# Kernel optimization log

Measured on AMD Instinct MI355X. Metric: run time of the kernel, lower is better.

## Reference

```python
import jax, jax.numpy as jnp
import numpy as np

N, K, C, OUT = 2048, 14, 512, 512
SCALE = 4.0
BN_EPS = 1e-5


def _edge_lists(k):
    # pairs i<j with i,j != k-1 and adj[i,j] > 0 (adj is fully connected ones)
    ei, ej = [], []
    for i in range(k - 1):
        for j in range(i + 1, k - 1):
            ei.append(i)
            ej.append(j)
    return np.asarray(ei, np.int32), np.asarray(ej, np.int32)


def setup_inputs() -> dict:
    key = jax.random.key(0)
    k0, k1, k2, k3 = jax.random.split(key, 4)
    ei, ej = _edge_lists(K)
    std = 0.02
    return {
        "inputs": jax.random.normal(k0, (N, K, C), dtype=jnp.float32),
        "adj": jnp.ones((K, K), dtype=jnp.float32),
        "edge_i": jnp.asarray(ei),
        "edge_j": jnp.asarray(ej),
        "gamma": jnp.ones((C,), dtype=jnp.float32),
        "beta": jnp.zeros((C,), dtype=jnp.float32),
        "w_direct": jax.random.normal(k1, (C,), dtype=jnp.float32) * std,
        "W_merged": jax.random.normal(k2, (OUT, C), dtype=jnp.float32) * std,
        "W_orig": jax.random.normal(k3, (OUT, C), dtype=jnp.float32) * std,
    }


def reference(inputs, adj, edge_i, edge_j, gamma, beta, w_direct, W_merged, W_orig):
    n, k, c = inputs.shape
    # --- learn_adj ---
    global_feat = inputs[:, k - 1 : k, :]                      # [N,1,c]
    distances = jnp.abs(inputs - global_feat)                  # [N,k,c]
    # pairwise gaps only on the static edge list (i<j, non-global, adj>0)
    gap = 15.0 * (distances[:, edge_i, :] - distances[:, edge_j, :])  # [N,E,c]
    # BatchNorm1d over channel c, batch stats over (N, E), biased variance
    mean = jnp.mean(gap, axis=(0, 1))
    var = jnp.mean(jnp.square(gap - mean), axis=(0, 1))
    bn = (gap - mean) * (gamma / jnp.sqrt(var + BN_EPS)) + beta        # [N,E,c]
    a = jax.nn.sigmoid(SCALE * jnp.einsum("nec,c->ne", bn, w_direct))  # [N,E]
    adj2 = jnp.ones((n, k, k), dtype=inputs.dtype)
    adj2 = adj2.at[:, edge_i, edge_j].set(2.0 * a)
    adj2 = adj2.at[:, edge_j, edge_i].set(2.0 * (1.0 - a))
    new_adj = adj2 * adj[None, :, :]
    norm = jnp.sum(jnp.abs(new_adj), axis=2, keepdims=True)    # L1 row norm
    new_adj = new_adj / jnp.maximum(norm, 1e-12)
    # --- graph conv ---
    agg = jnp.einsum("nij,njc->nic", new_adj, inputs)          # [N,k,c]
    merged = jax.nn.relu(jnp.einsum("nkc,oc->nko", agg, W_merged))
    original = jnp.einsum("nkc,oc->nko", inputs, W_orig)
    return merged + original
```

## Files before the change

kernel.cpp:

```cpp
#include <hip/hip_runtime.h>
#include <stdint.h>

#define K_NODES 14
#define C_DIM   512
#define OUT_DIM 512
#define N_EDGE  78

typedef float  f32x4  __attribute__((ext_vector_type(4)));
typedef __bf16 bf16x8 __attribute__((ext_vector_type(8)));

__device__ __forceinline__ unsigned short f2bf(float f) {
    unsigned int u = __builtin_bit_cast(unsigned int, f);
    unsigned int r = (u + 0x7fffu + ((u >> 16) & 1u)) >> 16;
    return (unsigned short)r;
}
__device__ __forceinline__ float bf2f(unsigned short s) {
    return __builtin_bit_cast(float, (unsigned int)s << 16);
}

__device__ __forceinline__ void async16(const void* g, void* l) {
    __builtin_amdgcn_global_load_lds(
        (const __attribute__((address_space(1))) unsigned int*)g,
        (__attribute__((address_space(3))) unsigned int*)l, 16, 0, 0);
}

__global__ __launch_bounds__(1024) void stats_partial(
    const float* __restrict__ x, float* __restrict__ part,
    unsigned short* __restrict__ xbf,
    const float* __restrict__ Wm, const float* __restrict__ Wo,
    unsigned short* __restrict__ wmbf, unsigned short* __restrict__ wobf)
{
    int t  = threadIdx.x;
    int q  = t & 127;
    int sn = t >> 7;
    int n  = blockIdx.x * 8 + sn;
    size_t base = (size_t)n * K_NODES * C_DIM + q * 4;

    f32x4 g = *(const f32x4*)(x + base + 13 * C_DIM);
    ushort4 gb; gb.x=f2bf(g.x); gb.y=f2bf(g.y); gb.z=f2bf(g.z); gb.w=f2bf(g.w);
    *(ushort4*)(xbf + base + 13 * C_DIM) = gb;

    float S10=0,S11=0,S12=0,S13=0, S20=0,S21=0,S22=0,S23=0, Sw0=0,Sw1=0,Sw2=0,Sw3=0;
    #pragma unroll
    for (int k = 0; k < 13; ++k) {
        f32x4 v = *(const f32x4*)(x + base + k * C_DIM);
        ushort4 vb; vb.x=f2bf(v.x); vb.y=f2bf(v.y); vb.z=f2bf(v.z); vb.w=f2bf(v.w);
        *(ushort4*)(xbf + base + k * C_DIM) = vb;
        float wk = (float)(12 - 2 * k);
        float d0=fabsf(v.x-g.x), d1=fabsf(v.y-g.y), d2=fabsf(v.z-g.z), d3=fabsf(v.w-g.w);
        S10+=d0; S11+=d1; S12+=d2; S13+=d3;
        S20+=d0*d0; S21+=d1*d1; S22+=d2*d2; S23+=d3*d3;
        Sw0+=wk*d0; Sw1+=wk*d1; Sw2+=wk*d2; Sw3+=wk*d3;
    }
    f32x4 as = (f32x4){15.f*Sw0, 15.f*Sw1, 15.f*Sw2, 15.f*Sw3};
    f32x4 aq = (f32x4){225.f*(13.f*S20 - S10*S10), 225.f*(13.f*S21 - S11*S11),
                       225.f*(13.f*S22 - S12*S12), 225.f*(13.f*S23 - S13*S13)};

    __shared__ f32x4 redS[8][128];
    __shared__ f32x4 redQ[8][128];
    redS[sn][q] = as;
    redQ[sn][q] = aq;
    __syncthreads();
    if (sn == 0) {
        f32x4 s = redS[0][q], z = redQ[0][q];
        #pragma unroll
        for (int r = 1; r < 8; ++r) { s += redS[r][q]; z += redQ[r][q]; }
        *(f32x4*)(part + (size_t)blockIdx.x * 1024 + q * 4)       = s;
        *(f32x4*)(part + (size_t)blockIdx.x * 1024 + 512 + q * 4) = z;
    }
    int i0 = blockIdx.x * 1024 + t;
    wmbf[i0] = f2bf(Wm[i0]);
    wobf[i0] = f2bf(Wo[i0]);
}

__global__ __launch_bounds__(256) void finalize_stats(
    const float* __restrict__ part, float inv_ne,
    const float* __restrict__ gamma, const float* __restrict__ beta,
    const float* __restrict__ wdir, float* __restrict__ u, float* __restrict__ bpart)
{
    int lane = threadIdx.x & 63;
    int wv   = threadIdx.x >> 6;
    int c    = blockIdx.x * 64 + lane;
    float s = 0.f, q = 0.f;
    #pragma unroll 8
    for (int r = wv; r < 256; r += 4) {
        s += part[(size_t)r * 1024 + c];
        q += part[(size_t)r * 1024 + 512 + c];
    }
    __shared__ float shs[4][64], shq[4][64];
    shs[wv][lane] = s; shq[wv][lane] = q;
    __syncthreads();
    if (wv == 0) {
        s = shs[0][lane] + shs[1][lane] + shs[2][lane] + shs[3][lane];
        q = shq[0][lane] + shq[1][lane] + shq[2][lane] + shq[3][lane];
        float mean = s * inv_ne;
        float var  = q * inv_ne - mean * mean;
        float sc   = gamma[c] / sqrtf(var + 1e-5f);
        u[c] = sc * wdir[c];
        float b = (beta[c] - mean * sc) * wdir[c];
        #pragma unroll
        for (int off = 1; off < 64; off <<= 1) b += __shfl_xor(b, off, 64);
        if (lane == 0) bpart[blockIdx.x] = b;
    }
}

__global__ __launch_bounds__(256) void fuse_graph(
    const unsigned short* __restrict__ xbf, const float* __restrict__ adj,
    const int* __restrict__ ei, const int* __restrict__ ej,
    const float* __restrict__ u, const float* __restrict__ bpart,
    unsigned short* __restrict__ aggbf)
{
    __shared__ float WL[2][196];
    __shared__ float Dp[2][2][13];
    __shared__ float invL[2][14];
    int wv = threadIdx.x >> 6, lane = threadIdx.x & 63;
    int sp = wv >> 1;
    int h  = wv & 1;
    int n  = blockIdx.x * 2 + sp;
    size_t base = (size_t)n * K_NODES * C_DIM + h * 256 + lane * 4;

    float xf[K_NODES][4];
    #pragma unroll
    for (int k = 0; k < K_NODES; ++k) {
        uint2 raw = *(const uint2*)(xbf + base + k * C_DIM);
        xf[k][0]=bf2f(raw.x&0xffff); xf[k][1]=bf2f(raw.x>>16);
        xf[k][2]=bf2f(raw.y&0xffff); xf[k][3]=bf2f(raw.y>>16);
    }
    f32x4 uv = *(const f32x4*)(u + h * 256 + lane * 4);

    #pragma unroll
    for (int k = 0; k < 13; ++k) {
        float p = fabsf(xf[k][0]-xf[13][0])*uv.x + fabsf(xf[k][1]-xf[13][1])*uv.y
                + fabsf(xf[k][2]-xf[13][2])*uv.z + fabsf(xf[k][3]-xf[13][3])*uv.w;
        #pragma unroll
        for (int off = 1; off < 64; off <<= 1) p += __shfl_xor(p, off, 64);
        if (lane == 0) Dp[sp][h][k] = p;
    }
    __syncthreads();

    if (h == 0) {
        float bc = 0.f;
        #pragma unroll
        for (int b8 = 0; b8 < 8; ++b8) bc += bpart[b8];
        for (int e = lane; e < N_EDGE; e += 64) {
            int ii = ei[e], jj = ej[e];
            float Di = Dp[sp][0][ii] + Dp[sp][1][ii];
            float Dj = Dp[sp][0][jj] + Dp[sp][1][jj];
            float z = 4.0f * (15.f * (Di - Dj) + bc);
            float a = 1.f / (1.f + expf(-z));
            WL[sp][ii * K_NODES + jj] = adj[ii * K_NODES + jj] * (2.f * a);
            WL[sp][jj * K_NODES + ii] = adj[jj * K_NODES + ii] * (2.f * (1.f - a));
        }
    } else {
        for (int idx = lane; idx < K_NODES * K_NODES; idx += 64) {
            int i = idx / K_NODES, j = idx - i * K_NODES;
            if (i == j || i == 13 || j == 13) WL[sp][idx] = adj[idx];
        }
    }
    __syncthreads();
    if (h == 0 && lane < K_NODES) {
        float s = 0.f;
        #pragma unroll
        for (int j = 0; j < K_NODES; ++j) s += fabsf(WL[sp][lane * K_NODES + j]);
        invL[sp][lane] = 1.f / fmaxf(s, 1e-12f);
    }
    __syncthreads();

    #pragma unroll
    for (int i = 0; i < K_NODES; ++i) {
        float s0=0.f,s1=0.f,s2=0.f,s3=0.f;
        #pragma unroll
        for (int j = 0; j < K_NODES; ++j) {
            float w = WL[sp][i * K_NODES + j];
            s0 += w*xf[j][0]; s1 += w*xf[j][1]; s2 += w*xf[j][2]; s3 += w*xf[j][3];
        }
        float wi = invL[sp][i];
        uint2 r;
        r.x = (unsigned int)f2bf(s0*wi) | ((unsigned int)f2bf(s1*wi) << 16);
        r.y = (unsigned int)f2bf(s2*wi) | ((unsigned int)f2bf(s3*wi) << 16);
        *(uint2*)(aggbf + base + i * C_DIM) = r;
    }
}

#define TM 128
#define TN 128
#define BK 64

__global__ __launch_bounds__(256) void gemm_fused(
    const unsigned short* __restrict__ Aagg, const unsigned short* __restrict__ Axin,
    const unsigned short* __restrict__ Bwm,  const unsigned short* __restrict__ Bwo,
    float* __restrict__ out)
{
    __shared__ unsigned short lA[2][TM * BK];
    __shared__ unsigned short lB[2][TN * BK];
    int tid  = threadIdx.x;
    int lane = tid & 63;
    int wave = tid >> 6;
    int wr = wave >> 1, wc = wave & 1;
    int bm = blockIdx.x * TM;
    int bn = blockIdx.y * TN;

    f32x4 acc[4][4];
    #pragma unroll
    for (int i = 0; i < 4; ++i)
        #pragma unroll
        for (int j = 0; j < 4; ++j) acc[i][j] = (f32x4){0.f, 0.f, 0.f, 0.f};

    int lrow = lane & 15;
    int xorv = lane & 7;
    int srow  = tid >> 3;
    int lcu   = ((tid & 7) ^ (srow & 7)) * 8;

#define STAGE(buf, Ap, Bp, kb)                                              \
    _Pragma("unroll")                                                        \
    for (int it = 0; it < 4; ++it) {                                         \
        int row = it * 32 + srow;                                            \
        async16((Ap) + (size_t)(bm + row) * C_DIM + (kb) + lcu,              \
                &lA[buf][(it * 256 + wave * 64) * 8]);                       \
        async16((Bp) + (size_t)(bn + row) * C_DIM + (kb) + lcu,              \
                &lB[buf][(it * 256 + wave * 64) * 8]);                       \
    }

    STAGE(0, Aagg, Bwm, 0);
    __syncthreads();

    #pragma unroll
    for (int ph = 0; ph < 16; ++ph) {
        const int cur = ph & 1;
        if (ph < 15) {
            const unsigned short* Ap = ((ph + 1) < 8) ? Aagg : Axin;
            const unsigned short* Bp = ((ph + 1) < 8) ? Bwm  : Bwo;
            STAGE(cur ^ 1, Ap, Bp, ((ph + 1) & 7) * BK);
        }
        #pragma unroll
        for (int ks = 0; ks < 2; ++ks) {
            int pchunk = ((ks * 4 + (lane >> 4)) ^ xorv) * 8;
            bf16x8 af[4], bfr[4];
            #pragma unroll
            for (int i = 0; i < 4; ++i)
                af[i] = *(const bf16x8*)&lA[cur][(wr * 64 + i * 16 + lrow) * BK + pchunk];
            #pragma unroll
            for (int j = 0; j < 4; ++j)
                bfr[j] = *(const bf16x8*)&lB[cur][(wc * 64 + j * 16 + lrow) * BK + pchunk];
            #pragma unroll
            for (int i = 0; i < 4; ++i)
                #pragma unroll
                for (int j = 0; j < 4; ++j)
                    acc[i][j] = __builtin_amdgcn_mfma_f32_16x16x32_bf16(
                        af[i], bfr[j], acc[i][j], 0, 0, 0);
        }
        if (ph == 7) {
            #pragma unroll
            for (int i = 0; i < 4; ++i)
                #pragma unroll
                for (int j = 0; j < 4; ++j)
                    #pragma unroll
                    for (int r = 0; r < 4; ++r)
                        acc[i][j][r] = fmaxf(acc[i][j][r], 0.f);
        }
        __syncthreads();
    }
#undef STAGE

    int orow0 = bm + wr * 64 + (lane >> 4) * 4;
    int ocol0 = bn + wc * 64 + (lane & 15);
    #pragma unroll
    for (int i = 0; i < 4; ++i)
        #pragma unroll
        for (int j = 0; j < 4; ++j)
            #pragma unroll
            for (int r = 0; r < 4; ++r)
                out[(size_t)(orow0 + i * 16 + r) * OUT_DIM + (ocol0 + j * 16)] = acc[i][j][r];
}

extern "C" void kernel_launch(void* const* d_in, const int* in_sizes, int n_in,
                              void* d_out, int out_size, void* d_ws, size_t ws_size,
                              hipStream_t stream)
{
    const float* x     = (const float*)d_in[0];
    const float* adj   = (const float*)d_in[1];
    const int*   ei    = (const int*)d_in[2];
    const int*   ej    = (const int*)d_in[3];
    const float* gamma = (const float*)d_in[4];
    const float* beta  = (const float*)d_in[5];
    const float* wdir  = (const float*)d_in[6];
    const float* Wm    = (const float*)d_in[7];
    const float* Wo    = (const float*)d_in[8];
    float* out = (float*)d_out;

    int N = in_sizes[0] / (K_NODES * C_DIM);
    int M = N * K_NODES;

    float* ws_f   = (float*)d_ws;
    float* u      = ws_f + 1024;
    float* bpart  = ws_f + 1536;
    float* part   = ws_f + 2048;
    char*  wsb    = (char*)d_ws;
    size_t off    = (size_t)(2048 + 256 * 1024) * sizeof(float);
    unsigned short* wmbf  = (unsigned short*)(wsb + off);  off += (size_t)OUT_DIM * C_DIM * 2;
    unsigned short* wobf  = (unsigned short*)(wsb + off);  off += (size_t)OUT_DIM * C_DIM * 2;
    unsigned short* xbf   = (unsigned short*)(wsb + off);  off += (size_t)M * C_DIM * 2;
    unsigned short* aggbf = (unsigned short*)(wsb + off);

    float inv_ne = 1.0f / ((float)N * (float)N_EDGE);

    hipLaunchKernelGGL(stats_partial, dim3(N / 8), dim3(1024), 0, stream,
                       x, part, xbf, Wm, Wo, wmbf, wobf);
    hipLaunchKernelGGL(finalize_stats, dim3(8), dim3(256), 0, stream,
                       part, inv_ne, gamma, beta, wdir, u, bpart);
    hipLaunchKernelGGL(fuse_graph, dim3(N / 2), dim3(256), 0, stream,
                       xbf, adj, ei, ej, u, bpart, aggbf);
    hipLaunchKernelGGL(gemm_fused, dim3(M / TM, OUT_DIM / TN), dim3(256), 0, stream,
                       aggbf, xbf, wmbf, wobf, out);
}
```

Baseline: 183.3 us.

## Rework stats/graph kernels' thread mapping and swizzle GEMM tile order

The stats kernel now uses 512 threads, each processing two samples, and converts twice as many weight elements. The graph kernel assigns one wave per sample with 8 channels per lane, which removes the block-level __syncthreads and the cross-wave partial sums. The GEMM launch becomes 1D with a remapped tile index that groups blocks by the 8 XCDs, for better L2 reuse of A rows. The main risks are lower occupancy from the larger register arrays and a hard-coded grid size (112) in the swizzle.

```diff
diff --git a/kernel.cpp b/kernel.cpp
--- a/kernel.cpp
+++ b/kernel.cpp
@@ -24,7 +24,7 @@
         (__attribute__((address_space(3))) unsigned int*)l, 16, 0, 0);
 }
 
-__global__ __launch_bounds__(1024) void stats_partial(
+__global__ __launch_bounds__(512) void stats_partial(
     const float* __restrict__ x, float* __restrict__ part,
     unsigned short* __restrict__ xbf,
     const float* __restrict__ Wm, const float* __restrict__ Wo,
@@ -33,44 +33,52 @@
     int t  = threadIdx.x;
     int q  = t & 127;
     int sn = t >> 7;
-    int n  = blockIdx.x * 8 + sn;
-    size_t base = (size_t)n * K_NODES * C_DIM + q * 4;
-
-    f32x4 g = *(const f32x4*)(x + base + 13 * C_DIM);
-    ushort4 gb; gb.x=f2bf(g.x); gb.y=f2bf(g.y); gb.z=f2bf(g.z); gb.w=f2bf(g.w);
-    *(ushort4*)(xbf + base + 13 * C_DIM) = gb;
-
-    float S10=0,S11=0,S12=0,S13=0, S20=0,S21=0,S22=0,S23=0, Sw0=0,Sw1=0,Sw2=0,Sw3=0;
-    #pragma unroll
-    for (int k = 0; k < 13; ++k) {
-        f32x4 v = *(const f32x4*)(x + base + k * C_DIM);
-        ushort4 vb; vb.x=f2bf(v.x); vb.y=f2bf(v.y); vb.z=f2bf(v.z); vb.w=f2bf(v.w);
-        *(ushort4*)(xbf + base + k * C_DIM) = vb;
-        float wk = (float)(12 - 2 * k);
-        float d0=fabsf(v.x-g.x), d1=fabsf(v.y-g.y), d2=fabsf(v.z-g.z), d3=fabsf(v.w-g.w);
-        S10+=d0; S11+=d1; S12+=d2; S13+=d3;
-        S20+=d0*d0; S21+=d1*d1; S22+=d2*d2; S23+=d3*d3;
-        Sw0+=wk*d0; Sw1+=wk*d1; Sw2+=wk*d2; Sw3+=wk*d3;
-    }
-    f32x4 as = (f32x4){15.f*Sw0, 15.f*Sw1, 15.f*Sw2, 15.f*Sw3};
-    f32x4 aq = (f32x4){225.f*(13.f*S20 - S10*S10), 225.f*(13.f*S21 - S11*S11),
-                       225.f*(13.f*S22 - S12*S12), 225.f*(13.f*S23 - S13*S13)};
-
-    __shared__ f32x4 redS[8][128];
-    __shared__ f32x4 redQ[8][128];
+    f32x4 as = (f32x4){0.f,0.f,0.f,0.f};
+    f32x4 aq = (f32x4){0.f,0.f,0.f,0.f};
+
+    #pragma unroll
+    for (int half = 0; half < 2; ++half) {
+        int n = blockIdx.x * 8 + half * 4 + sn;
+        size_t base = (size_t)n * K_NODES * C_DIM + q * 4;
+
+        f32x4 g = *(const f32x4*)(x + base + 13 * C_DIM);
+        ushort4 gb; gb.x=f2bf(g.x); gb.y=f2bf(g.y); gb.z=f2bf(g.z); gb.w=f2bf(g.w);
+        *(ushort4*)(xbf + base + 13 * C_DIM) = gb;
+
+        float S10=0,S11=0,S12=0,S13=0, S20=0,S21=0,S22=0,S23=0, Sw0=0,Sw1=0,Sw2=0,Sw3=0;
+        #pragma unroll
+        for (int k = 0; k < 13; ++k) {
+            f32x4 v = *(const f32x4*)(x + base + k * C_DIM);
+            ushort4 vb; vb.x=f2bf(v.x); vb.y=f2bf(v.y); vb.z=f2bf(v.z); vb.w=f2bf(v.w);
+            *(ushort4*)(xbf + base + k * C_DIM) = vb;
+            float wk = (float)(12 - 2 * k);
+            float d0=fabsf(v.x-g.x), d1=fabsf(v.y-g.y), d2=fabsf(v.z-g.z), d3=fabsf(v.w-g.w);
+            S10+=d0; S11+=d1; S12+=d2; S13+=d3;
+            S20+=d0*d0; S21+=d1*d1; S22+=d2*d2; S23+=d3*d3;
+            Sw0+=wk*d0; Sw1+=wk*d1; Sw2+=wk*d2; Sw3+=wk*d3;
+        }
+        as += (f32x4){15.f*Sw0, 15.f*Sw1, 15.f*Sw2, 15.f*Sw3};
+        aq += (f32x4){225.f*(13.f*S20 - S10*S10), 225.f*(13.f*S21 - S11*S11),
+                      225.f*(13.f*S22 - S12*S12), 225.f*(13.f*S23 - S13*S13)};
+    }
+
+    __shared__ f32x4 redS[4][128];
+    __shared__ f32x4 redQ[4][128];
     redS[sn][q] = as;
     redQ[sn][q] = aq;
     __syncthreads();
     if (sn == 0) {
         f32x4 s = redS[0][q], z = redQ[0][q];
         #pragma unroll
-        for (int r = 1; r < 8; ++r) { s += redS[r][q]; z += redQ[r][q]; }
+        for (int r = 1; r < 4; ++r) { s += redS[r][q]; z += redQ[r][q]; }
         *(f32x4*)(part + (size_t)blockIdx.x * 1024 + q * 4)       = s;
         *(f32x4*)(part + (size_t)blockIdx.x * 1024 + 512 + q * 4) = z;
     }
     int i0 = blockIdx.x * 1024 + t;
     wmbf[i0] = f2bf(Wm[i0]);
     wobf[i0] = f2bf(Wo[i0]);
+    wmbf[i0 + 512] = f2bf(Wm[i0 + 512]);
+    wobf[i0 + 512] = f2bf(Wo[i0 + 512]);
 }
 
 __global__ __launch_bounds__(256) void finalize_stats(
@@ -110,75 +118,85 @@
     const float* __restrict__ u, const float* __restrict__ bpart,
     unsigned short* __restrict__ aggbf)
 {
-    __shared__ float WL[2][196];
-    __shared__ float Dp[2][2][13];
-    __shared__ float invL[2][14];
+    __shared__ float WL[4][196];
+    __shared__ float Dsh[4][13];
+    __shared__ float invW[4][14];
     int wv = threadIdx.x >> 6, lane = threadIdx.x & 63;
-    int sp = wv >> 1;
-    int h  = wv & 1;
-    int n  = blockIdx.x * 2 + sp;
-    size_t base = (size_t)n * K_NODES * C_DIM + h * 256 + lane * 4;
-
-    float xf[K_NODES][4];
+    int n  = blockIdx.x * 4 + wv;
+    size_t base = (size_t)n * K_NODES * C_DIM + lane * 8;
+
+    float xf[K_NODES][8];
     #pragma unroll
     for (int k = 0; k < K_NODES; ++k) {
-        uint2 raw = *(const uint2*)(xbf + base + k * C_DIM);
+        uint4 raw = *(const uint4*)(xbf + base + k * C_DIM);
         xf[k][0]=bf2f(raw.x&0xffff); xf[k][1]=bf2f(raw.x>>16);
         xf[k][2]=bf2f(raw.y&0xffff); xf[k][3]=bf2f(raw.y>>16);
-    }
-    f32x4 uv = *(const f32x4*)(u + h * 256 + lane * 4);
+        xf[k][4]=bf2f(raw.z&0xffff); xf[k][5]=bf2f(raw.z>>16);
+        xf[k][6]=bf2f(raw.w&0xffff); xf[k][7]=bf2f(raw.w>>16);
+    }
+    float uvv[8];
+    {
+        f32x4 a = *(const f32x4*)(u + lane * 8);
+        f32x4 b = *(const f32x4*)(u + lane * 8 + 4);
+        uvv[0]=a.x; uvv[1]=a.y; uvv[2]=a.z; uvv[3]=a.w;
+        uvv[4]=b.x; uvv[5]=b.y; uvv[6]=b.z; uvv[7]=b.w;
+    }
 
     #pragma unroll
     for (int k = 0; k < 13; ++k) {
-        float p = fabsf(xf[k][0]-xf[13][0])*uv.x + fabsf(xf[k][1]-xf[13][1])*uv.y
-                + fabsf(xf[k][2]-xf[13][2])*uv.z + fabsf(xf[k][3]-xf[13][3])*uv.w;
+        float p = 0.f;
+        #pragma unroll
+        for (int c = 0; c < 8; ++c) p += fabsf(xf[k][c]-xf[13][c])*uvv[c];
         #pragma unroll
         for (int off = 1; off < 64; off <<= 1) p += __shfl_xor(p, off, 64);
-        if (lane == 0) Dp[sp][h][k] = p;
-    }
-    __syncthreads();
-
-    if (h == 0) {
-        float bc = 0.f;
-        #pragma unroll
-        for (int b8 = 0; b8 < 8; ++b8) bc += bpart[b8];
-        for (int e = lane; e < N_EDGE; e += 64) {
+        if (lane == 0) Dsh[wv][k] = p;
+    }
+
+    #pragma unroll
+    for (int r = 0; r < 4; ++r) {
+        int idx = r * 64 + lane;
+        if (idx < K_NODES * K_NODES) {
+            int i = idx / K_NODES, j = idx - i * K_NODES;
+            if (i == j || i == 13 || j == 13) WL[wv][idx] = adj[idx];
+        }
+    }
+    float bc = 0.f;
+    #pragma unroll
+    for (int b8 = 0; b8 < 8; ++b8) bc += bpart[b8];
+    #pragma unroll
+    for (int r = 0; r < 2; ++r) {
+        int e = r * 64 + lane;
+        if (e < N_EDGE) {
             int ii = ei[e], jj = ej[e];
-            float Di = Dp[sp][0][ii] + Dp[sp][1][ii];
-            float Dj = Dp[sp][0][jj] + Dp[sp][1][jj];
-            float z = 4.0f * (15.f * (Di - Dj) + bc);
+            float z = 4.0f * (15.f * (Dsh[wv][ii] - Dsh[wv][jj]) + bc);
             float a = 1.f / (1.f + expf(-z));
-            WL[sp][ii * K_NODES + jj] = adj[ii * K_NODES + jj] * (2.f * a);
-            WL[sp][jj * K_NODES + ii] = adj[jj * K_NODES + ii] * (2.f * (1.f - a));
-        }
-    } else {
-        for (int idx = lane; idx < K_NODES * K_NODES; idx += 64) {
-            int i = idx / K_NODES, j = idx - i * K_NODES;
-            if (i == j || i == 13 || j == 13) WL[sp][idx] = adj[idx];
-        }
-    }
-    __syncthreads();
-    if (h == 0 && lane < K_NODES) {
+            WL[wv][ii * K_NODES + jj] = adj[ii * K_NODES + jj] * (2.f * a);
+            WL[wv][jj * K_NODES + ii] = adj[jj * K_NODES + ii] * (2.f * (1.f - a));
+        }
+    }
+    if (lane < K_NODES) {
         float s = 0.f;
         #pragma unroll
-        for (int j = 0; j < K_NODES; ++j) s += fabsf(WL[sp][lane * K_NODES + j]);
-        invL[sp][lane] = 1.f / fmaxf(s, 1e-12f);
-    }
-    __syncthreads();
+        for (int j = 0; j < K_NODES; ++j) s += fabsf(WL[wv][lane * K_NODES + j]);
+        invW[wv][lane] = 1.f / fmaxf(s, 1e-12f);
+    }
 
     #pragma unroll
     for (int i = 0; i < K_NODES; ++i) {
-        float s0=0.f,s1=0.f,s2=0.f,s3=0.f;
+        float s0=0,s1=0,s2=0,s3=0,s4=0,s5=0,s6=0,s7=0;
         #pragma unroll
         for (int j = 0; j < K_NODES; ++j) {
-            float w = WL[sp][i * K_NODES + j];
-            s0 += w*xf[j][0]; s1 += w*xf[j][1]; s2 += w*xf[j][2]; s3 += w*xf[j][3];
-        }
-        float wi = invL[sp][i];
-        uint2 r;
+            float w = WL[wv][i * K_NODES + j];
+            s0+=w*xf[j][0]; s1+=w*xf[j][1]; s2+=w*xf[j][2]; s3+=w*xf[j][3];
+            s4+=w*xf[j][4]; s5+=w*xf[j][5]; s6+=w*xf[j][6]; s7+=w*xf[j][7];
+        }
+        float wi = invW[wv][i];
+        uint4 r;
         r.x = (unsigned int)f2bf(s0*wi) | ((unsigned int)f2bf(s1*wi) << 16);
         r.y = (unsigned int)f2bf(s2*wi) | ((unsigned int)f2bf(s3*wi) << 16);
-        *(uint2*)(aggbf + base + i * C_DIM) = r;
+        r.z = (unsigned int)f2bf(s4*wi) | ((unsigned int)f2bf(s5*wi) << 16);
+        r.w = (unsigned int)f2bf(s6*wi) | ((unsigned int)f2bf(s7*wi) << 16);
+        *(uint4*)(aggbf + base + i * C_DIM) = r;
     }
 }
 
@@ -197,8 +215,10 @@
     int lane = tid & 63;
     int wave = tid >> 6;
     int wr = wave >> 1, wc = wave & 1;
-    int bm = blockIdx.x * TM;
-    int bn = blockIdx.y * TN;
+    int lin = blockIdx.x;
+    int g   = (lin & 7) * 112 + (lin >> 3);
+    int bm  = (g >> 2) * TM;
+    int bn  = (g & 3)  * TN;
 
     f32x4 acc[4][4];
     #pragma unroll
@@ -304,12 +324,12 @@
 
     float inv_ne = 1.0f / ((float)N * (float)N_EDGE);
 
-    hipLaunchKernelGGL(stats_partial, dim3(N / 8), dim3(1024), 0, stream,
+    hipLaunchKernelGGL(stats_partial, dim3(N / 8), dim3(512), 0, stream,
                        x, part, xbf, Wm, Wo, wmbf, wobf);
     hipLaunchKernelGGL(finalize_stats, dim3(8), dim3(256), 0, stream,
                        part, inv_ne, gamma, beta, wdir, u, bpart);
-    hipLaunchKernelGGL(fuse_graph, dim3(N / 2), dim3(256), 0, stream,
+    hipLaunchKernelGGL(fuse_graph, dim3(N / 4), dim3(256), 0, stream,
                        xbf, adj, ei, ej, u, bpart, aggbf);
-    hipLaunchKernelGGL(gemm_fused, dim3(M / TM, OUT_DIM / TN), dim3(256), 0, stream,
+    hipLaunchKernelGGL(gemm_fused, dim3((M / TM) * (OUT_DIM / TN)), dim3(256), 0, stream,
                        aggbf, xbf, wmbf, wobf, out);
 }
```

After: 180.9 us. Within noise of the previous version (-1.3%).
